# Performance work log

Measured on AMD Instinct MI355X. Metric: run time of the kernel, lower is better.

The kernel has to match this reference:

```python
import jax, jax.numpy as jnp
import numpy as np
from jax import lax

EPS = 1e-6


def layernorm2d(x, w, b):
    # channel LayerNorm over dim C of NCHW (biased variance), matching LayerNormFunction
    mu = jnp.mean(x, axis=1, keepdims=True)
    var = jnp.mean((x - mu) ** 2, axis=1, keepdims=True)
    y = (x - mu) * lax.rsqrt(var + EPS)
    return w[None, :, None, None] * y + b[None, :, None, None]


def conv1x1(x, W, b):
    # x: (N,C,H,W), W: (O,C), b: (O,)
    return jnp.einsum('nchw,oc->nohw', x, W) + b[None, :, None, None]


def conv3x3(x, W, b):
    # W: (O,I,3,3)
    y = lax.conv_general_dilated(x, W, window_strides=(1, 1), padding='SAME',
                                 dimension_numbers=('NCHW', 'OIHW', 'NCHW'))
    return y + b[None, :, None, None]


def avg_pool3x3(x):
    # torch F.avg_pool2d k=3, s=1, p=1, count_include_pad=True -> always divide by 9
    s = lax.reduce_window(x, 0.0, lax.add, (1, 1, 3, 3), (1, 1, 1, 1),
                          [(0, 0), (0, 0), (1, 1), (1, 1)])
    return s / 9.0


def setup_inputs() -> dict:
    key = jax.random.key(0)
    N, C, H, W = 8, 64, 128, 256
    ks = jax.random.split(key, 12)
    d = {
        'x_l': jax.random.normal(ks[0], (N, C, H, W), jnp.float32),
        'x_r': jax.random.normal(ks[1], (N, C, H, W), jnp.float32),
        'nl_w': jnp.ones((C,), jnp.float32),
        'nl_b': jnp.zeros((C,), jnp.float32),
        'nr_w': jnp.ones((C,), jnp.float32),
        'nr_b': jnp.zeros((C,), jnp.float32),
        'Wq_l': jax.random.normal(ks[2], (C, C), jnp.float32) * 0.05,
        'bq_l': jax.random.normal(ks[3], (C,), jnp.float32) * 0.05,
        'Wq_r': jax.random.normal(ks[4], (C, C), jnp.float32) * 0.05,
        'bq_r': jax.random.normal(ks[5], (C,), jnp.float32) * 0.05,
        'Wv_r': jax.random.normal(ks[6], (C, C), jnp.float32) * 0.05,
        'bv_r': jax.random.normal(ks[7], (C,), jnp.float32) * 0.05,
        'beta': jax.random.normal(ks[8], (1, C, 1, 1), jnp.float32) * 0.1,
        'gamma': jax.random.normal(ks[9], (1, C, 1, 1), jnp.float32) * 0.1,
        'W_hf': jax.random.normal(ks[10], (C, C, 3, 3), jnp.float32) * 0.02,
        'b_hf': jax.random.normal(ks[11], (C,), jnp.float32) * 0.02,
    }
    return d


def reference(x_l, x_r, nl_w, nl_b, nr_w, nr_b, Wq_l, bq_l, Wq_r, bq_r,
              Wv_r, bv_r, beta, gamma, W_hf, b_hf):
    C = x_l.shape[1]
    scale = C ** (-0.5)

    # Projections (1x1 convs); Q_l, Q_r, V_r as (N,H,W,C)
    Q_l = jnp.transpose(conv1x1(layernorm2d(x_l, nl_w, nl_b), Wq_l, bq_l), (0, 2, 3, 1))
    Q_r = jnp.transpose(conv1x1(layernorm2d(x_r, nr_w, nr_b), Wq_r, bq_r), (0, 2, 3, 1))
    V_r = jnp.transpose(conv1x1(x_r, Wv_r, bv_r), (0, 2, 3, 1))

    # Per-scanline cross attention: (N,H,W,W)
    attn = jnp.einsum('nhwc,nhvc->nhwv', Q_l, Q_r) * scale
    attn = jax.nn.softmax(attn, axis=-1)
    F_r2l = jnp.einsum('nhwv,nhvc->nhwc', attn, V_r)  # (N,H,W,C)
    F_r2l = jnp.transpose(F_r2l, (0, 3, 1, 2)) * beta  # (N,C,H,W)

    # High-frequency branch
    hf = conv3x3(x_r - avg_pool3x3(x_r), W_hf, b_hf)

    return x_l + F_r2l + gamma * hf
```

## Files before the change

kernel.cpp:

```cpp
#include <hip/hip_runtime.h>
#include <hip/hip_bf16.h>

#define N_ 8
#define C_ 64
#define H_ 128
#define W_ 256
#define HW_ (H_*W_)
#define CHW_ (C_*H_*W_)

typedef unsigned int u32;
typedef unsigned short u16;
typedef float f32x4 __attribute__((ext_vector_type(4)));
typedef short bf16x8 __attribute__((ext_vector_type(8)));

__device__ __forceinline__ float blo(u32 u) { return __uint_as_float(u << 16); }
__device__ __forceinline__ float bhi(u32 u) { return __uint_as_float(u & 0xffff0000u); }
__device__ __forceinline__ u16 f2bf(float f) {
    u32 u = __float_as_uint(f);
    u32 lsb = (u >> 16) & 1u;
    u += 0x7fffu + lsb;
    return (u16)(u >> 16);
}
__device__ __forceinline__ u32 pack2(float a, float b) {
    return (u32)f2bf(a) | ((u32)f2bf(b) << 16);
}
__device__ __forceinline__ int rmap(int px) {
    return (px & 0xF8) | ((px + (px >> 3)) & 7);
}

__global__ __launch_bounds__(256) void k_fused(
    const float* __restrict__ xl, const float* __restrict__ xr,
    const float* __restrict__ nlw, const float* __restrict__ nlb,
    const float* __restrict__ nrw, const float* __restrict__ nrb,
    const float* __restrict__ Wql, const float* __restrict__ bql,
    const float* __restrict__ Wqr, const float* __restrict__ bqr,
    const float* __restrict__ Wvr, const float* __restrict__ bvr,
    const float* __restrict__ beta, float* __restrict__ out)
{
    __shared__ u32 B1[8192];
    __shared__ u32 B2[8192];
    __shared__ uint4 Ks[2048];
    __shared__ float muA[256], rsA[256];
    __shared__ float SlA[64], BlA[64], SrA[64], BrA[64], BvA[64];
    const int tid  = threadIdx.x;
    const int lane = tid & 63, wv = tid >> 6;
    const int l15  = lane & 15, kg = lane >> 4;
    const int blk  = blockIdx.x;
    const int n = blk >> 7, h = blk & 127;
    const size_t gbase = (size_t)n*CHW_ + (size_t)h*W_;

    if (tid < 64) {
        const int o = tid;
        float sl = 0.f, bl = bql[o], sr = 0.f, br = bqr[o];
        for (int c = 0; c < 64; ++c) {
            float wl = Wql[o*64+c], wr = Wqr[o*64+c];
            sl += wl * nlw[c];
            bl += wl * nlb[c];
            sr += wr * nrw[c];
            br += wr * nrb[c];
        }
        SlA[o] = sl; BlA[o] = bl; SrA[o] = sr; BrA[o] = br; BvA[o] = bvr[o];
    }

    const int oA = wv*16 + l15;
    bf16x8 aL[2], aR[2], aV[2];
    #pragma unroll
    for (int hf = 0; hf < 2; ++hf) {
        bf16x8 tl, tr, tv;
        #pragma unroll
        for (int j = 0; j < 8; ++j) {
            const int c = hf*32 + kg*8 + j;
            tl[j] = (short)f2bf(Wql[oA*64+c] * nlw[c]);
            tr[j] = (short)f2bf(Wqr[oA*64+c] * nrw[c]);
            tv[j] = (short)f2bf(Wvr[oA*64+c]);
        }
        aL[hf] = tl; aR[hf] = tr; aV[hf] = tv;
    }

    #pragma unroll
    for (int it2 = 0; it2 < 2; ++it2) {
        const int g = it2*256 + tid;
        const int chunk = g >> 6;
        const int j = g & 63;
        const int c0 = chunk*8;
        float4 v[8];
        #pragma unroll
        for (int e = 0; e < 8; ++e)
            v[e] = *(const float4*)(xl + gbase + (size_t)(c0+e)*HW_ + j*4);
        #pragma unroll
        for (int t = 0; t < 4; ++t) {
            const int px = j*4 + t;
            const int r = rmap(px);
            u32 q0,q1,q2,q3;
            const float* f0 = (const float*)&v[0]; const float* f1 = (const float*)&v[1];
            const float* f2 = (const float*)&v[2]; const float* f3 = (const float*)&v[3];
            const float* f4 = (const float*)&v[4]; const float* f5 = (const float*)&v[5];
            const float* f6 = (const float*)&v[6]; const float* f7 = (const float*)&v[7];
            asm("v_cvt_pk_bf16_f32 %0, %1, %2" : "=v"(q0) : "v"(f0[t]), "v"(f1[t]));
            asm("v_cvt_pk_bf16_f32 %0, %1, %2" : "=v"(q1) : "v"(f2[t]), "v"(f3[t]));
            asm("v_cvt_pk_bf16_f32 %0, %1, %2" : "=v"(q2) : "v"(f4[t]), "v"(f5[t]));
            asm("v_cvt_pk_bf16_f32 %0, %1, %2" : "=v"(q3) : "v"(f6[t]), "v"(f7[t]));
            uint4 pv; pv.x=q0; pv.y=q1; pv.z=q2; pv.w=q3;
            *(uint4*)&B1[r*32 + ((chunk ^ (r&7))<<2)] = pv;
        }
    }
    __syncthreads();
    {
        const int px = tid & 255;
        const int r = rmap(px);
        float sum = 0.f, ssq = 0.f;
        #pragma unroll
        for (int c8 = 0; c8 < 8; ++c8) {
            uint4 val = *(const uint4*)&B1[r*32 + ((c8 ^ (r&7))<<2)];
            const u32* wp = (const u32*)&val;
            #pragma unroll
            for (int q = 0; q < 4; ++q) {
                float a = blo(wp[q]), b = bhi(wp[q]);
                sum += a + b; ssq += a*a + b*b;
            }
        }
        float mu = sum * (1.f/64.f);
        float var = ssq * (1.f/64.f) - mu*mu;
        muA[px] = mu;
        rsA[px] = rsqrtf(var + 1e-6f);
    }
    __syncthreads();
    {
        float Sv[4], Bv[4];
        #pragma unroll
        for (int r4 = 0; r4 < 4; ++r4) {
            Sv[r4] = SlA[wv*16 + kg*4 + r4];
            Bv[r4] = BlA[wv*16 + kg*4 + r4];
        }
        #pragma unroll
        for (int nt = 0; nt < 16; ++nt) {
            const int px = nt*16 + l15;
            const int r = rmap(px);
            f32x4 d = {0.f,0.f,0.f,0.f};
            #pragma unroll
            for (int hf = 0; hf < 2; ++hf) {
                bf16x8 b = *(const bf16x8*)&B1[r*32 + (((hf*4+kg) ^ (r&7))<<2)];
                d = __builtin_amdgcn_mfma_f32_16x16x32_bf16(aL[hf], b, d, 0, 0, 0);
            }
            const float mu = muA[px], rs = rsA[px];
            uint2 pv;
            pv.x = pack2(rs*(d[0] - mu*Sv[0]) + Bv[0], rs*(d[1] - mu*Sv[1]) + Bv[1]);
            pv.y = pack2(rs*(d[2] - mu*Sv[2]) + Bv[2], rs*(d[3] - mu*Sv[3]) + Bv[3]);
            const int ci = (wv*2 + (kg>>1)) ^ (px & 7);
            *(uint2*)&B2[px*32 + (ci<<2) + (kg&1)*2] = pv;
        }
    }
    __syncthreads();

    bf16x8 qf[4][2];
    #pragma unroll
    for (int ntq = 0; ntq < 4; ++ntq)
        #pragma unroll
        for (int ci = 0; ci < 2; ++ci) {
            const int q = wv*64 + ntq*16 + l15;
            qf[ntq][ci] = *(const bf16x8*)&B2[q*32 + (((ci*4+kg) ^ (q&7))<<2)];
        }
    #pragma unroll
    for (int it2 = 0; it2 < 2; ++it2) {
        const int g = it2*256 + tid;
        const int chunk = g >> 6;
        const int j = g & 63;
        const int c0 = chunk*8;
        float4 v[8];
        #pragma unroll
        for (int e = 0; e < 8; ++e)
            v[e] = *(const float4*)(xr + gbase + (size_t)(c0+e)*HW_ + j*4);
        #pragma unroll
        for (int t = 0; t < 4; ++t) {
            const int px = j*4 + t;
            const int r = rmap(px);
            u32 q0,q1,q2,q3;
            const float* f0 = (const float*)&v[0]; const float* f1 = (const float*)&v[1];
            const float* f2 = (const float*)&v[2]; const float* f3 = (const float*)&v[3];
            const float* f4 = (const float*)&v[4]; const float* f5 = (const float*)&v[5];
            const float* f6 = (const float*)&v[6]; const float* f7 = (const float*)&v[7];
            asm("v_cvt_pk_bf16_f32 %0, %1, %2" : "=v"(q0) : "v"(f0[t]), "v"(f1[t]));
            asm("v_cvt_pk_bf16_f32 %0, %1, %2" : "=v"(q1) : "v"(f2[t]), "v"(f3[t]));
            asm("v_cvt_pk_bf16_f32 %0, %1, %2" : "=v"(q2) : "v"(f4[t]), "v"(f5[t]));
            asm("v_cvt_pk_bf16_f32 %0, %1, %2" : "=v"(q3) : "v"(f6[t]), "v"(f7[t]));
            uint4 pv; pv.x=q0; pv.y=q1; pv.z=q2; pv.w=q3;
            *(uint4*)&B1[r*32 + ((chunk ^ (r&7))<<2)] = pv;
        }
    }
    __syncthreads();
    {
        const int px = tid & 255;
        const int r = rmap(px);
        float sum = 0.f, ssq = 0.f;
        #pragma unroll
        for (int c8 = 0; c8 < 8; ++c8) {
            uint4 val = *(const uint4*)&B1[r*32 + ((c8 ^ (r&7))<<2)];
            const u32* wp = (const u32*)&val;
            #pragma unroll
            for (int q = 0; q < 4; ++q) {
                float a = blo(wp[q]), b = bhi(wp[q]);
                sum += a + b; ssq += a*a + b*b;
            }
        }
        float mu = sum * (1.f/64.f);
        float var = ssq * (1.f/64.f) - mu*mu;
        muA[px] = mu;
        rsA[px] = rsqrtf(var + 1e-6f);
    }
    __syncthreads();
    {
        float Sv[4], Bv[4];
        #pragma unroll
        for (int r4 = 0; r4 < 4; ++r4) {
            Sv[r4] = SrA[wv*16 + kg*4 + r4];
            Bv[r4] = BrA[wv*16 + kg*4 + r4];
        }
        const int chv = wv*16 + l15;
        const float vbias = BvA[chv];
        u32* KsW = (u32*)Ks;
        u16* Vts = (u16*)B2;
        #pragma unroll
        for (int nt = 0; nt < 16; ++nt) {
            const int px = nt*16 + l15;
            const int r = rmap(px);
            bf16x8 bX[2];
            #pragma unroll
            for (int hf = 0; hf < 2; ++hf)
                bX[hf] = *(const bf16x8*)&B1[r*32 + (((hf*4+kg) ^ (r&7))<<2)];
            f32x4 dq = {0.f,0.f,0.f,0.f};
            f32x4 dv = {0.f,0.f,0.f,0.f};
            #pragma unroll
            for (int hf = 0; hf < 2; ++hf) {
                dq = __builtin_amdgcn_mfma_f32_16x16x32_bf16(aR[hf], bX[hf], dq, 0, 0, 0);
                dv = __builtin_amdgcn_mfma_f32_16x16x32_bf16(bX[hf], aV[hf], dv, 0, 0, 0);
            }
            const float mu = muA[px], rs = rsA[px];
            uint2 pq;
            pq.x = pack2(rs*(dq[0] - mu*Sv[0]) + Bv[0], rs*(dq[1] - mu*Sv[1]) + Bv[1]);
            pq.y = pack2(rs*(dq[2] - mu*Sv[2]) + Bv[2], rs*(dq[3] - mu*Sv[3]) + Bv[3]);
            const int ciq = (wv*2 + (kg>>1)) ^ (px & 7);
            *(uint2*)&KsW[px*32 + (ciq<<2) + (kg&1)*2] = pq;
            uint2 pw;
            pw.x = pack2(dv[0] + vbias, dv[1] + vbias);
            pw.y = pack2(dv[2] + vbias, dv[3] + vbias);
            const int swz = (nt*2 + (kg>>1)) ^ (chv & 7);
            *(uint2*)&Vts[chv*256 + (swz<<3) + (kg&1)*4] = pw;
        }
    }
    __syncthreads();

    f32x4 oacc[4][4];
    #pragma unroll
    for (int a = 0; a < 4; ++a)
        #pragma unroll
        for (int b = 0; b < 4; ++b)
            oacc[a][b] = (f32x4){0.f,0.f,0.f,0.f};
    float lsum[4] = {0.f,0.f,0.f,0.f};
    u32* Pw = &B1[wv*1024];
    const u16* Vts = (const u16*)B2;
    const int q0 = wv*64;

    for (int kb = 0; kb < 8; ++kb) {
        f32x4 st[2][4];
        #pragma unroll
        for (int mt = 0; mt < 2; ++mt)
            #pragma unroll
            for (int nt = 0; nt < 4; ++nt)
                st[mt][nt] = (f32x4){0.f,0.f,0.f,0.f};
        #pragma unroll
        for (int ci = 0; ci < 2; ++ci) {
            bf16x8 a0 = *(const bf16x8*)&Ks[(kb*32 +      l15)*8 + ((ci*4 + kg) ^ (l15 & 7))];
            bf16x8 a1 = *(const bf16x8*)&Ks[(kb*32 + 16 + l15)*8 + ((ci*4 + kg) ^ (l15 & 7))];
            #pragma unroll
            for (int nt = 0; nt < 4; ++nt) {
                st[0][nt] = __builtin_amdgcn_mfma_f32_16x16x32_bf16(a0, qf[nt][ci], st[0][nt], 0, 0, 0);
                st[1][nt] = __builtin_amdgcn_mfma_f32_16x16x32_bf16(a1, qf[nt][ci], st[1][nt], 0, 0, 0);
            }
        }
        #pragma unroll
        for (int nt = 0; nt < 4; ++nt) {
            const int q = nt*16 + l15;
            #pragma unroll
            for (int mt = 0; mt < 2; ++mt) {
                float p0 = __expf(st[mt][nt][0]*0.125f);
                float p1 = __expf(st[mt][nt][1]*0.125f);
                float p2 = __expf(st[mt][nt][2]*0.125f);
                float p3 = __expf(st[mt][nt][3]*0.125f);
                lsum[nt] += (p0+p1)+(p2+p3);
                u32 pr0, pr1;
                asm("v_cvt_pk_bf16_f32 %0, %1, %2" : "=v"(pr0) : "v"(p0), "v"(p1));
                asm("v_cvt_pk_bf16_f32 %0, %1, %2" : "=v"(pr1) : "v"(p2), "v"(p3));
                const int c16 = (2*mt + (kg >> 1)) ^ (q & 3);
                uint2 pv; pv.x = pr0; pv.y = pr1;
                *(uint2*)&Pw[q*16 + c16*4 + (kg & 1)*2] = pv;
            }
        }
        asm volatile("s_waitcnt lgkmcnt(0)" ::: "memory");
        bf16x8 vb[4];
        #pragma unroll
        for (int nc = 0; nc < 4; ++nc)
            vb[nc] = *(const bf16x8*)&Vts[(nc*16 + l15)*256 + ((kb*4 + kg) ^ (l15 & 7))*8];
        #pragma unroll
        for (int qt = 0; qt < 4; ++qt) {
            const int q = qt*16 + l15;
            bf16x8 pa = *(const bf16x8*)&Pw[q*16 + (kg ^ (q & 3))*4];
            #pragma unroll
            for (int nc = 0; nc < 4; ++nc)
                oacc[qt][nc] = __builtin_amdgcn_mfma_f32_16x16x32_bf16(pa, vb[nc], oacc[qt][nc], 0, 0, 0);
        }
    }

    #pragma unroll
    for (int nt = 0; nt < 4; ++nt) {
        float s = lsum[nt];
        s += __shfl_xor(s, 16, 64);
        s += __shfl_xor(s, 32, 64);
        lsum[nt] = s;
    }
    float linv[4][4];
    #pragma unroll
    for (int qt = 0; qt < 4; ++qt)
        #pragma unroll
        for (int r = 0; r < 4; ++r)
            linv[qt][r] = 1.0f / __shfl(lsum[qt], kg*4 + r, 64);

    float* PwF = (float*)Pw;
    const size_t obase = (size_t)n*CHW_ + (size_t)h*W_ + q0;
    #pragma unroll
    for (int nc = 0; nc < 4; ++nc) {
        asm volatile("s_waitcnt lgkmcnt(0)" ::: "memory");
        #pragma unroll
        for (int qt = 0; qt < 4; ++qt) {
            f32x4 vals;
            vals[0] = oacc[qt][nc][0]*linv[qt][0];
            vals[1] = oacc[qt][nc][1]*linv[qt][1];
            vals[2] = oacc[qt][nc][2]*linv[qt][2];
            vals[3] = oacc[qt][nc][3]*linv[qt][3];
            *(f32x4*)&PwF[l15*64 + ((qt*4 + kg) ^ l15)*4] = vals;
        }
        asm volatile("s_waitcnt lgkmcnt(0)" ::: "memory");
        #pragma unroll
        for (int chl = 0; chl < 16; ++chl) {
            const int ch = nc*16 + chl;
            float v = PwF[chl*64 + ((lane >> 2) ^ chl)*4 + (lane & 3)];
            size_t gidx = obase + (size_t)ch*HW_ + lane;
            float prev = out[gidx];
            out[gidx] = xl[gidx] + beta[ch]*v + prev;
        }
    }
}

__global__ __launch_bounds__(256) void k_hipass(
    const float* __restrict__ xr, u16* __restrict__ Tt)
{
    __shared__ u16 Ts[64*256];
    const int bid = blockIdx.x;
    const int blk = (bid & 7)*128 + (bid >> 3);
    const int n = blk >> 7, h = blk & 127;
    const int tid = threadIdx.x;
    const int lane = tid & 63, wv = tid >> 6;
    const float* rowp = xr + (size_t)n*CHW_ + (size_t)h*W_ + lane*4;

    #pragma unroll
    for (int ci = 0; ci < 16; ++ci) {
        const int c = wv*16 + ci;
        const float* pc = rowp + (size_t)c*HW_;
        float ctr0=0.f, ctr1=0.f, ctr2=0.f, ctr3=0.f;
        float s0=0.f, s1=0.f, s2=0.f, s3=0.f;
        #pragma unroll
        for (int dy = -1; dy <= 1; ++dy) {
            const int hh = h + dy;
            float4 v = {0.f,0.f,0.f,0.f};
            if (hh >= 0 && hh < 128) v = *(const float4*)(pc + dy*W_);
            float lft = __shfl_up(v.w, 1);
            float rgt = __shfl_down(v.x, 1);
            if (lane == 0)  lft = 0.f;
            if (lane == 63) rgt = 0.f;
            s0 += lft + v.x + v.y;
            s1 += v.x + v.y + v.z;
            s2 += v.y + v.z + v.w;
            s3 += v.z + v.w + rgt;
            if (dy == 0) { ctr0=v.x; ctr1=v.y; ctr2=v.z; ctr3=v.w; }
        }
        uint2 pv;
        pv.x = pack2(ctr0 - s0*(1.f/9.f), ctr1 - s1*(1.f/9.f));
        pv.y = pack2(ctr2 - s2*(1.f/9.f), ctr3 - s3*(1.f/9.f));
        const int swz = (c >> 3) << 3;
        *(uint2*)&Ts[c*256 + ((lane*4) ^ swz)] = pv;
    }
    __syncthreads();
    uint4* gout = (uint4*)(Tt + (size_t)blk*256*64);
    #pragma unroll
    for (int iter = 0; iter < 8; ++iter) {
        const int lin = iter*256 + tid;
        const int px = lin >> 3, chunk = lin & 7;
        const int pxs = px ^ (chunk << 3);
        u32 w4[4];
        #pragma unroll
        for (int tp = 0; tp < 4; ++tp) {
            const int c0 = chunk*8 + tp*2;
            u16 a = Ts[(c0    )*256 + pxs];
            u16 b = Ts[(c0 + 1)*256 + pxs];
            w4[tp] = (u32)a | ((u32)b << 16);
        }
        uint4 v; v.x=w4[0]; v.y=w4[1]; v.z=w4[2]; v.w=w4[3];
        gout[lin] = v;
    }
}

__device__ __forceinline__ void conv_tile(
    const uint4* __restrict__ buf, const bf16x8* A,
    const float* gv, const float* bv,
    int n, int h, int w0, int mt, int l15, int kg,
    float* __restrict__ out)
{
    f32x4 acc[4] = {{0,0,0,0},{0,0,0,0},{0,0,0,0},{0,0,0,0}};
    #pragma unroll
    for (int s = 0; s < 18; ++s) {
        const int q  = s >> 1;
        const int dy = q / 3, dx = q % 3;
        const int c0 = (s & 1)*4 + kg;
        #pragma unroll
        for (int nt = 0; nt < 4; ++nt) {
            const int wt = nt*16 + l15 + dx;
            bf16x8 b = *(const bf16x8*)&buf[(dy*66 + wt)*8 + (c0 ^ (wt & 7))];
            acc[nt] = __builtin_amdgcn_mfma_f32_16x16x32_bf16(A[s], b, acc[nt], 0, 0, 0);
        }
    }
    #pragma unroll
    for (int nt = 0; nt < 4; ++nt) {
        const int px = w0 + nt*16 + l15;
        #pragma unroll
        for (int r = 0; r < 4; ++r) {
            const int oo = mt*16 + kg*4 + r;
            size_t idx = (size_t)(n*64 + oo)*HW_ + (size_t)h*W_ + px;
            out[idx] = gv[r]*(acc[nt][r] + bv[r]);
        }
    }
}

__global__ __launch_bounds__(256) void k_conv(
    const u16* __restrict__ Tt, const float* __restrict__ Whf,
    const float* __restrict__ bhf, const float* __restrict__ gam,
    float* __restrict__ out)
{
    __shared__ uint4 Xs[2][1584];
    const int tid  = threadIdx.x;
    const int lane = tid & 63;
    const int mt   = tid >> 6;
    const int l15  = lane & 15;
    const int kg   = lane >> 4;
    const int bid  = blockIdx.x;
    const int blk2 = (bid & 7)*256 + (bid >> 3);
    const int row  = blk2 >> 1, half = blk2 & 1;
    const int n = row >> 7, h = row & 127;
    const int w00 = half*128;
    const int w01 = w00 + 64;

    const int oa = mt*16 + l15;
    bf16x8 A[18];
    #pragma unroll
    for (int s = 0; s < 18; ++s) {
        const int q  = s >> 1;
        const int ib = (s & 1)*32 + kg*8;
        bf16x8 a;
        #pragma unroll
        for (int j = 0; j < 8; ++j) {
            float wv = Whf[(size_t)(oa*64 + ib + j)*9 + q];
            a[j] = (short)f2bf(wv);
        }
        A[s] = a;
    }
    float gv[4], bv[4];
    #pragma unroll
    for (int r = 0; r < 4; ++r) {
        int oo = mt*16 + kg*4 + r;
        gv[r] = gam[oo];
        bv[r] = bhf[oo];
    }

    for (int it = tid; it < 1584; it += 256) {
        int dy    = it / 528;
        int rem   = it - dy*528;
        int wt    = rem >> 3;
        int chunk = rem & 7;
        int hh = h + dy - 1;
        int wg = w00 + wt - 1;
        uint4 v = {0,0,0,0};
        if (hh >= 0 && hh < 128 && wg >= 0 && wg < 256)
            v = *(const uint4*)(Tt + (((size_t)(n*128 + hh)*256 + wg)*64 + chunk*8));
        Xs[0][(dy*66 + wt)*8 + (chunk ^ (wt & 7))] = v;
    }
    __syncthreads();

    uint4 rr[7];
    #pragma unroll
    for (int k = 0; k < 7; ++k) {
        const int it = k*256 + tid;
        if (it < 1584) {
            int dy    = it / 528;
            int rem   = it - dy*528;
            int wt    = rem >> 3;
            int chunk = rem & 7;
            int hh = h + dy - 1;
            int wg = w01 + wt - 1;
            uint4 v = {0,0,0,0};
            if (hh >= 0 && hh < 128 && wg >= 0 && wg < 256)
                v = *(const uint4*)(Tt + (((size_t)(n*128 + hh)*256 + wg)*64 + chunk*8));
            rr[k] = v;
        }
    }

    conv_tile(&Xs[0][0], A, gv, bv, n, h, w00, mt, l15, kg, out);

    #pragma unroll
    for (int k = 0; k < 7; ++k) {
        const int it = k*256 + tid;
        if (it < 1584) {
            int dy    = it / 528;
            int rem   = it - dy*528;
            int wt    = rem >> 3;
            int chunk = rem & 7;
            Xs[1][(dy*66 + wt)*8 + (chunk ^ (wt & 7))] = rr[k];
        }
    }
    __syncthreads();
    conv_tile(&Xs[1][0], A, gv, bv, n, h, w01, mt, l15, kg, out);
}

extern "C" void kernel_launch(void* const* d_in, const int* in_sizes, int n_in,
                              void* d_out, int out_size, void* d_ws, size_t ws_size,
                              hipStream_t stream)
{
    const float* xl   = (const float*)d_in[0];
    const float* xr   = (const float*)d_in[1];
    const float* nlw  = (const float*)d_in[2];
    const float* nlb  = (const float*)d_in[3];
    const float* nrw  = (const float*)d_in[4];
    const float* nrb  = (const float*)d_in[5];
    const float* Wql  = (const float*)d_in[6];
    const float* bql  = (const float*)d_in[7];
    const float* Wqr  = (const float*)d_in[8];
    const float* bqr  = (const float*)d_in[9];
    const float* Wvr  = (const float*)d_in[10];
    const float* bvr  = (const float*)d_in[11];
    const float* beta = (const float*)d_in[12];
    const float* gam  = (const float*)d_in[13];
    const float* Whf  = (const float*)d_in[14];
    const float* bhf  = (const float*)d_in[15];
    float* out = (float*)d_out;

    u16* Tt = (u16*)d_ws;

    k_hipass<<<1024, 256, 0, stream>>>(xr, Tt);
    k_conv<<<2048, 256, 0, stream>>>(Tt, Whf, bhf, gam, out);
    k_fused<<<1024, 256, 0, stream>>>(xl, xr, nlw, nlb, nrw, nrb,
                                      Wql, bql, Wqr, bqr, Wvr, bvr,
                                      beta, out);
}
```

Baseline: 194.3 us.

## Double k_fused block to 512 threads, splitting query and pixel work across eight waves

The fused attention kernel now launches 512 threads per block (eight wavefronts) instead of 256. Each wave handles half as many pixel tiles in the projection stages and 32 queries instead of 64 in the attention loop. The epilogue is remapped to write 32-query rows with a new swizzle. This raises per-block parallelism and cuts per-thread register use, which may help latency hiding. In exchange, each wave redundantly reloads the K and V fragments, and at most one block of this size may fit per CU because of the large LDS footprint.

```diff
diff --git a/kernel.cpp b/kernel.cpp
--- a/kernel.cpp
+++ b/kernel.cpp
@@ -28,7 +28,7 @@
     return (px & 0xF8) | ((px + (px >> 3)) & 7);
 }
 
-__global__ __launch_bounds__(256) void k_fused(
+__global__ __launch_bounds__(512) void k_fused(
     const float* __restrict__ xl, const float* __restrict__ xr,
     const float* __restrict__ nlw, const float* __restrict__ nlb,
     const float* __restrict__ nrw, const float* __restrict__ nrb,
@@ -45,6 +45,8 @@
     const int tid  = threadIdx.x;
     const int lane = tid & 63, wv = tid >> 6;
     const int l15  = lane & 15, kg = lane >> 4;
+    const int mw   = wv & 3;
+    const int nh   = wv >> 2;
     const int blk  = blockIdx.x;
     const int n = blk >> 7, h = blk & 127;
     const size_t gbase = (size_t)n*CHW_ + (size_t)h*W_;
@@ -62,7 +64,7 @@
         SlA[o] = sl; BlA[o] = bl; SrA[o] = sr; BrA[o] = br; BvA[o] = bvr[o];
     }
 
-    const int oA = wv*16 + l15;
+    const int oA = mw*16 + l15;
     bf16x8 aL[2], aR[2], aV[2];
     #pragma unroll
     for (int hf = 0; hf < 2; ++hf) {
@@ -77,11 +79,9 @@
         aL[hf] = tl; aR[hf] = tr; aV[hf] = tv;
     }
 
-    #pragma unroll
-    for (int it2 = 0; it2 < 2; ++it2) {
-        const int g = it2*256 + tid;
-        const int chunk = g >> 6;
-        const int j = g & 63;
+    {
+        const int chunk = tid >> 6;
+        const int j = tid & 63;
         const int c0 = chunk*8;
         float4 v[8];
         #pragma unroll
@@ -105,8 +105,8 @@
         }
     }
     __syncthreads();
-    {
-        const int px = tid & 255;
+    if (tid < 256) {
+        const int px = tid;
         const int r = rmap(px);
         float sum = 0.f, ssq = 0.f;
         #pragma unroll
@@ -129,11 +129,12 @@
         float Sv[4], Bv[4];
         #pragma unroll
         for (int r4 = 0; r4 < 4; ++r4) {
-            Sv[r4] = SlA[wv*16 + kg*4 + r4];
-            Bv[r4] = BlA[wv*16 + kg*4 + r4];
-        }
-        #pragma unroll
-        for (int nt = 0; nt < 16; ++nt) {
+            Sv[r4] = SlA[mw*16 + kg*4 + r4];
+            Bv[r4] = BlA[mw*16 + kg*4 + r4];
+        }
+        #pragma unroll
+        for (int nt2 = 0; nt2 < 8; ++nt2) {
+            const int nt = nh*8 + nt2;
             const int px = nt*16 + l15;
             const int r = rmap(px);
             f32x4 d = {0.f,0.f,0.f,0.f};
@@ -146,25 +147,23 @@
             uint2 pv;
             pv.x = pack2(rs*(d[0] - mu*Sv[0]) + Bv[0], rs*(d[1] - mu*Sv[1]) + Bv[1]);
             pv.y = pack2(rs*(d[2] - mu*Sv[2]) + Bv[2], rs*(d[3] - mu*Sv[3]) + Bv[3]);
-            const int ci = (wv*2 + (kg>>1)) ^ (px & 7);
+            const int ci = (mw*2 + (kg>>1)) ^ (px & 7);
             *(uint2*)&B2[px*32 + (ci<<2) + (kg&1)*2] = pv;
         }
     }
     __syncthreads();
 
-    bf16x8 qf[4][2];
-    #pragma unroll
-    for (int ntq = 0; ntq < 4; ++ntq)
+    bf16x8 qf[2][2];
+    #pragma unroll
+    for (int ntq = 0; ntq < 2; ++ntq)
         #pragma unroll
         for (int ci = 0; ci < 2; ++ci) {
-            const int q = wv*64 + ntq*16 + l15;
+            const int q = wv*32 + ntq*16 + l15;
             qf[ntq][ci] = *(const bf16x8*)&B2[q*32 + (((ci*4+kg) ^ (q&7))<<2)];
         }
-    #pragma unroll
-    for (int it2 = 0; it2 < 2; ++it2) {
-        const int g = it2*256 + tid;
-        const int chunk = g >> 6;
-        const int j = g & 63;
+    {
+        const int chunk = tid >> 6;
+        const int j = tid & 63;
         const int c0 = chunk*8;
         float4 v[8];
         #pragma unroll
@@ -188,8 +187,8 @@
         }
     }
     __syncthreads();
-    {
-        const int px = tid & 255;
+    if (tid < 256) {
+        const int px = tid;
         const int r = rmap(px);
         float sum = 0.f, ssq = 0.f;
         #pragma unroll
@@ -212,15 +211,16 @@
         float Sv[4], Bv[4];
         #pragma unroll
         for (int r4 = 0; r4 < 4; ++r4) {
-            Sv[r4] = SrA[wv*16 + kg*4 + r4];
-            Bv[r4] = BrA[wv*16 + kg*4 + r4];
-        }
-        const int chv = wv*16 + l15;
+            Sv[r4] = SrA[mw*16 + kg*4 + r4];
+            Bv[r4] = BrA[mw*16 + kg*4 + r4];
+        }
+        const int chv = mw*16 + l15;
         const float vbias = BvA[chv];
         u32* KsW = (u32*)Ks;
         u16* Vts = (u16*)B2;
         #pragma unroll
-        for (int nt = 0; nt < 16; ++nt) {
+        for (int nt2 = 0; nt2 < 8; ++nt2) {
+            const int nt = nh*8 + nt2;
             const int px = nt*16 + l15;
             const int r = rmap(px);
             bf16x8 bX[2];
@@ -238,7 +238,7 @@
             uint2 pq;
             pq.x = pack2(rs*(dq[0] - mu*Sv[0]) + Bv[0], rs*(dq[1] - mu*Sv[1]) + Bv[1]);
             pq.y = pack2(rs*(dq[2] - mu*Sv[2]) + Bv[2], rs*(dq[3] - mu*Sv[3]) + Bv[3]);
-            const int ciq = (wv*2 + (kg>>1)) ^ (px & 7);
+            const int ciq = (mw*2 + (kg>>1)) ^ (px & 7);
             *(uint2*)&KsW[px*32 + (ciq<<2) + (kg&1)*2] = pq;
             uint2 pw;
             pw.x = pack2(dv[0] + vbias, dv[1] + vbias);
@@ -249,37 +249,36 @@
     }
     __syncthreads();
 
-    f32x4 oacc[4][4];
-    #pragma unroll
-    for (int a = 0; a < 4; ++a)
+    f32x4 oacc[2][4];
+    #pragma unroll
+    for (int a = 0; a < 2; ++a)
         #pragma unroll
         for (int b = 0; b < 4; ++b)
             oacc[a][b] = (f32x4){0.f,0.f,0.f,0.f};
-    float lsum[4] = {0.f,0.f,0.f,0.f};
-    u32* Pw = &B1[wv*1024];
+    float lsum[2] = {0.f,0.f};
+    u32* Pw = &B1[wv*512];
     const u16* Vts = (const u16*)B2;
-    const int q0 = wv*64;
 
     for (int kb = 0; kb < 8; ++kb) {
-        f32x4 st[2][4];
+        f32x4 st[2][2];
         #pragma unroll
         for (int mt = 0; mt < 2; ++mt)
             #pragma unroll
-            for (int nt = 0; nt < 4; ++nt)
+            for (int nt = 0; nt < 2; ++nt)
                 st[mt][nt] = (f32x4){0.f,0.f,0.f,0.f};
         #pragma unroll
         for (int ci = 0; ci < 2; ++ci) {
             bf16x8 a0 = *(const bf16x8*)&Ks[(kb*32 +      l15)*8 + ((ci*4 + kg) ^ (l15 & 7))];
             bf16x8 a1 = *(const bf16x8*)&Ks[(kb*32 + 16 + l15)*8 + ((ci*4 + kg) ^ (l15 & 7))];
             #pragma unroll
-            for (int nt = 0; nt < 4; ++nt) {
+            for (int nt = 0; nt < 2; ++nt) {
                 st[0][nt] = __builtin_amdgcn_mfma_f32_16x16x32_bf16(a0, qf[nt][ci], st[0][nt], 0, 0, 0);
                 st[1][nt] = __builtin_amdgcn_mfma_f32_16x16x32_bf16(a1, qf[nt][ci], st[1][nt], 0, 0, 0);
             }
         }
         #pragma unroll
-        for (int nt = 0; nt < 4; ++nt) {
-            const int q = nt*16 + l15;
+        for (int nt = 0; nt < 2; ++nt) {
+            const int ql = nt*16 + l15;
             #pragma unroll
             for (int mt = 0; mt < 2; ++mt) {
                 float p0 = __expf(st[mt][nt][0]*0.125f);
@@ -290,9 +289,9 @@
                 u32 pr0, pr1;
                 asm("v_cvt_pk_bf16_f32 %0, %1, %2" : "=v"(pr0) : "v"(p0), "v"(p1));
                 asm("v_cvt_pk_bf16_f32 %0, %1, %2" : "=v"(pr1) : "v"(p2), "v"(p3));
-                const int c16 = (2*mt + (kg >> 1)) ^ (q & 3);
+                const int c16 = (2*mt + (kg >> 1)) ^ (ql & 3);
                 uint2 pv; pv.x = pr0; pv.y = pr1;
-                *(uint2*)&Pw[q*16 + c16*4 + (kg & 1)*2] = pv;
+                *(uint2*)&Pw[ql*16 + c16*4 + (kg & 1)*2] = pv;
             }
         }
         asm volatile("s_waitcnt lgkmcnt(0)" ::: "memory");
@@ -301,9 +300,9 @@
         for (int nc = 0; nc < 4; ++nc)
             vb[nc] = *(const bf16x8*)&Vts[(nc*16 + l15)*256 + ((kb*4 + kg) ^ (l15 & 7))*8];
         #pragma unroll
-        for (int qt = 0; qt < 4; ++qt) {
-            const int q = qt*16 + l15;
-            bf16x8 pa = *(const bf16x8*)&Pw[q*16 + (kg ^ (q & 3))*4];
+        for (int qt = 0; qt < 2; ++qt) {
+            const int ql = qt*16 + l15;
+            bf16x8 pa = *(const bf16x8*)&Pw[ql*16 + (kg ^ (ql & 3))*4];
             #pragma unroll
             for (int nc = 0; nc < 4; ++nc)
                 oacc[qt][nc] = __builtin_amdgcn_mfma_f32_16x16x32_bf16(pa, vb[nc], oacc[qt][nc], 0, 0, 0);
@@ -311,41 +310,42 @@
     }
 
     #pragma unroll
-    for (int nt = 0; nt < 4; ++nt) {
+    for (int nt = 0; nt < 2; ++nt) {
         float s = lsum[nt];
         s += __shfl_xor(s, 16, 64);
         s += __shfl_xor(s, 32, 64);
         lsum[nt] = s;
     }
-    float linv[4][4];
-    #pragma unroll
-    for (int qt = 0; qt < 4; ++qt)
+    float linv[2][4];
+    #pragma unroll
+    for (int qt = 0; qt < 2; ++qt)
         #pragma unroll
         for (int r = 0; r < 4; ++r)
             linv[qt][r] = 1.0f / __shfl(lsum[qt], kg*4 + r, 64);
 
     float* PwF = (float*)Pw;
-    const size_t obase = (size_t)n*CHW_ + (size_t)h*W_ + q0;
+    const size_t obase = gbase + wv*32;
     #pragma unroll
     for (int nc = 0; nc < 4; ++nc) {
         asm volatile("s_waitcnt lgkmcnt(0)" ::: "memory");
         #pragma unroll
-        for (int qt = 0; qt < 4; ++qt) {
+        for (int qt = 0; qt < 2; ++qt) {
             f32x4 vals;
             vals[0] = oacc[qt][nc][0]*linv[qt][0];
             vals[1] = oacc[qt][nc][1]*linv[qt][1];
             vals[2] = oacc[qt][nc][2]*linv[qt][2];
             vals[3] = oacc[qt][nc][3]*linv[qt][3];
-            *(f32x4*)&PwF[l15*64 + ((qt*4 + kg) ^ l15)*4] = vals;
+            *(f32x4*)&PwF[l15*32 + (((qt*4 + kg) ^ (l15 & 7))<<2)] = vals;
         }
         asm volatile("s_waitcnt lgkmcnt(0)" ::: "memory");
         #pragma unroll
-        for (int chl = 0; chl < 16; ++chl) {
-            const int ch = nc*16 + chl;
-            float v = PwF[chl*64 + ((lane >> 2) ^ chl)*4 + (lane & 3)];
-            size_t gidx = obase + (size_t)ch*HW_ + lane;
-            float prev = out[gidx];
-            out[gidx] = xl[gidx] + beta[ch]*v + prev;
+        for (int it = 0; it < 8; ++it) {
+            const int csub = it*2 + (lane >> 5);
+            const int qloc = lane & 31;
+            float v = PwF[csub*32 + ((((qloc >> 2)) ^ (csub & 7))<<2) + (qloc & 3)];
+            const int ch = nc*16 + csub;
+            size_t gidx = obase + (size_t)ch*HW_ + qloc;
+            out[gidx] = xl[gidx] + beta[ch]*v + out[gidx];
         }
     }
 }
@@ -554,7 +554,7 @@
 
     k_hipass<<<1024, 256, 0, stream>>>(xr, Tt);
     k_conv<<<2048, 256, 0, stream>>>(Tt, Whf, bhf, gam, out);
-    k_fused<<<1024, 256, 0, stream>>>(xl, xr, nlw, nlb, nrw, nrb,
+    k_fused<<<1024, 512, 0, stream>>>(xl, xr, nlw, nlb, nrw, nrb,
                                       Wql, bql, Wqr, bqr, Wvr, bvr,
                                       beta, out);
 }
```

Result: faster. 176.5 us (-9.1%).
